# Kernel optimization log

Hardware: AMD Instinct MI355X
Metric: run time of the kernel (lower is better)

The kernel has to match this reference:

```python
import jax, jax.numpy as jnp
import numpy as np

B, C_IN, C_OUT, D, H, W = 2, 128, 128, 16, 32, 32


def setup_inputs() -> dict:
    key = jax.random.key(0)
    kx, kw, kb = jax.random.split(key, 3)
    x = jax.random.normal(kx, (B, C_IN, D, H, W), dtype=jnp.float32)
    # ddpm_conv3x3 -> Conv3d(in_ch, out_ch, kernel=3, padding=1) with default (scaled-variance) init
    fan_in = C_IN * 3 * 3 * 3
    scale = 1.0 / np.sqrt(fan_in)
    Wk = jax.random.uniform(kw, (C_OUT, C_IN, 3, 3, 3), dtype=jnp.float32, minval=-scale, maxval=scale)
    b = jnp.zeros((C_OUT,), dtype=jnp.float32)
    return {"x": x, "Wk": Wk, "b": b}


def reference(x, Wk, b):
    h = jnp.repeat(jnp.repeat(jnp.repeat(x, 2, axis=2), 2, axis=3), 2, axis=4)
    # 3x3x3 conv, stride 1, padding 1 (SAME)
    out = jax.lax.conv_general_dilated(
        h, Wk,
        window_strides=(1, 1, 1),
        padding="SAME",
        dimension_numbers=("NCDHW", "OIDHW", "NCDHW"),
    )
    return out + b[None, :, None, None, None]
```

## Files before the change

### kernel.cpp

```cpp
#include <hip/hip_runtime.h>
#include <hip/hip_bf16.h>

#define B_    2
#define CIN   128
#define COUT  128
#define DD    16
#define HH    32
#define WW    32
#define XS_CI (DD*HH*WW)
#define XS_B  (CIN*XS_CI)
#define OS_H2 64
#define OS_D2 (64*64)
#define OS_CO (32*64*64)
#define OS_B  (COUT*OS_CO)

typedef __attribute__((ext_vector_type(8))) short   short8;
typedef __attribute__((ext_vector_type(4))) float   floatx4;

static __device__ __forceinline__ unsigned short f2bf(float f) {
    union { __hip_bfloat16 h; unsigned short u; } cv;
    cv.h = __float2bfloat16(f);
    return cv.u;
}

__global__ __launch_bounds__(256) void fold_kernel(const float* __restrict__ Wk,
                                                   unsigned short* __restrict__ Afold) {
    const int t = blockIdx.x * 256 + threadIdx.x;
    const int p  = t >> 14;
    const int ks = (t >> 9) & 31;
    const int ct = (t >> 6) & 7;
    const int l  = t & 63;
    const int co = ct * 16 + (l & 15);
    const int ci = ks * 4 + (l >> 4);
    const int ed = (p >> 2) & 1, eh = (p >> 1) & 1, ew = p & 1;

    const float* w = Wk + (co * CIN + ci) * 27;
    float wv[27];
    #pragma unroll
    for (int i = 0; i < 27; ++i) wv[i] = w[i];

    short8 pk;
    #pragma unroll
    for (int tt = 0; tt < 8; ++tt) {
        const int td = (tt >> 2) & 1, th = (tt >> 1) & 1, tw = tt & 1;
        const int dlo = ed ? (td ? 2 : 0) : (td ? 1 : 0);
        const int dhi = ed ? (td ? 2 : 1) : (td ? 2 : 0);
        const int hlo = eh ? (th ? 2 : 0) : (th ? 1 : 0);
        const int hhi = eh ? (th ? 2 : 1) : (th ? 2 : 0);
        const int wlo = ew ? (tw ? 2 : 0) : (tw ? 1 : 0);
        const int whi = ew ? (tw ? 2 : 1) : (tw ? 2 : 0);
        float s = 0.f;
        for (int kd = dlo; kd <= dhi; ++kd)
            for (int kh = hlo; kh <= hhi; ++kh)
                for (int kw = wlo; kw <= whi; ++kw)
                    s += wv[kd * 9 + kh * 3 + kw];
        pk[tt] = (short)f2bf(s);
    }
    reinterpret_cast<short8*>(Afold)[t] = pk;
}

__global__ __launch_bounds__(256) void upconv_mfma(const float* __restrict__ x,
                                                   const unsigned short* __restrict__ Afold,
                                                   const float* __restrict__ bias,
                                                   float* __restrict__ out) {
    __shared__ short Bt[2][128 * 64];
    char* buf0 = reinterpret_cast<char*>(&Bt[0][0]);
    char* buf1 = reinterpret_cast<char*>(&Bt[1][0]);

    const int tid  = threadIdx.x;
    const int wave = tid >> 6;
    const int lane = tid & 63;

    const int d      = blockIdx.x >> 3;
    const int h_base = (blockIdx.x & 7) * 4;
    const int p      = blockIdx.y;
    const int b      = blockIdx.z;
    const int ed = (p >> 2) & 1, eh = (p >> 1) & 1, ew = p & 1;

    const int n_s  = tid & 127;
    const int cils = tid >> 7;
    const int hs   = h_base + (n_s >> 5);
    const int ws_  = n_s & 31;
    const int d0 = d + ed - 1, h0 = hs + eh - 1, w0 = ws_ + ew - 1;

    int  off[8];
    bool ok[8];
    #pragma unroll
    for (int tt = 0; tt < 8; ++tt) {
        const int td = (tt >> 2) & 1, th = (tt >> 1) & 1, tw = tt & 1;
        const int dd2 = d0 + td, hh2 = h0 + th, ww2 = w0 + tw;
        ok[tt]  = ((unsigned)dd2 < DD) && ((unsigned)hh2 < HH) && ((unsigned)ww2 < WW);
        off[tt] = dd2 * (HH * WW) + hh2 * WW + ww2;
    }
    const int sw    = (n_s & 7) << 4;
    const int wbase = n_s * 128;
    const float* xb = x + (size_t)b * XS_B;

    const int co0 = (wave >> 1) * 64;
    const int n0  = (wave & 1) * 64;
    const int ct0 = (wave >> 1) * 4;

    floatx4 acc[4][4];
    #pragma unroll
    for (int i = 0; i < 4; ++i)
        #pragma unroll
        for (int j = 0; j < 4; ++j)
            acc[i][j] = (floatx4){0.f, 0.f, 0.f, 0.f};

    const short8* Ap = reinterpret_cast<const short8*>(Afold);

    float raw[4][8];

    auto gather = [&](int kc) {
        #pragma unroll
        for (int i = 0; i < 4; ++i) {
            const float* xc = xb + (size_t)(kc * 8 + cils + 2 * i) * XS_CI;
            #pragma unroll
            for (int tt = 0; tt < 8; ++tt)
                raw[i][tt] = ok[tt] ? xc[off[tt]] : 0.f;
        }
    };

    auto body = [&](int kc, char* bufc, bool last) {
        short8 a[2][4];
        #pragma unroll
        for (int ksl = 0; ksl < 2; ++ksl)
            #pragma unroll
            for (int ct = 0; ct < 4; ++ct)
                a[ksl][ct] = Ap[((size_t)((p * 32 + kc * 2 + ksl) * 8 + ct0 + ct)) * 64 + lane];

        #pragma unroll
        for (int i = 0; i < 4; ++i) {
            short8 pk;
            #pragma unroll
            for (int tt = 0; tt < 8; ++tt) pk[tt] = (short)f2bf(raw[i][tt]);
            *reinterpret_cast<short8*>(bufc + wbase + (((cils + 2 * i) * 16) ^ sw)) = pk;
        }

        if (!last) gather(kc + 1);

        asm volatile("s_waitcnt lgkmcnt(0)\n\ts_barrier" ::: "memory");

        __builtin_amdgcn_s_setprio(1);
        #pragma unroll
        for (int ksl = 0; ksl < 2; ++ksl) {
            short8 bfr[4];
            #pragma unroll
            for (int nt = 0; nt < 4; ++nt) {
                const int n  = n0 + nt * 16 + (lane & 15);
                const int kb = ksl * 64 + (lane >> 4) * 16;
                bfr[nt] = *reinterpret_cast<const short8*>(
                    bufc + n * 128 + (kb ^ ((n & 7) << 4)));
            }
            #pragma unroll
            for (int ct = 0; ct < 4; ++ct)
                #pragma unroll
                for (int nt = 0; nt < 4; ++nt)
                    acc[ct][nt] = __builtin_amdgcn_mfma_f32_16x16x32_bf16(
                        a[ksl][ct], bfr[nt], acc[ct][nt], 0, 0, 0);
        }
        __builtin_amdgcn_s_setprio(0);
    };

    gather(0);
    for (int kc = 0; kc < 16; kc += 2) {
        body(kc,     buf0, false);
        body(kc + 1, buf1, (kc + 1) == 15);
    }

    float* ob = out + (size_t)b * OS_B + (size_t)(2 * d + ed) * OS_D2;
    #pragma unroll
    for (int ct = 0; ct < 4; ++ct) {
        #pragma unroll
        for (int j = 0; j < 4; ++j) {
            const int co = co0 + ct * 16 + (lane >> 4) * 4 + j;
            const float bv = bias[co];
            #pragma unroll
            for (int nt = 0; nt < 4; ++nt) {
                const int n  = n0 + nt * 16 + (lane & 15);
                const int hl = n >> 5, wl = n & 31;
                const int h2 = 2 * (h_base + hl) + eh;
                const int w2 = 2 * wl + ew;
                ob[(size_t)co * OS_CO + h2 * OS_H2 + w2] = acc[ct][nt][j] + bv;
            }
        }
    }
}

extern "C" void kernel_launch(void* const* d_in, const int* in_sizes, int n_in,
                              void* d_out, int out_size, void* d_ws, size_t ws_size,
                              hipStream_t stream) {
    const float* x    = (const float*)d_in[0];
    const float* Wk   = (const float*)d_in[1];
    const float* bias = (const float*)d_in[2];
    float* out        = (float*)d_out;
    unsigned short* Afold = (unsigned short*)d_ws;

    fold_kernel<<<512, 256, 0, stream>>>(Wk, Afold);
    dim3 grid(DD * 8, 8, B_);
    upconv_mfma<<<grid, 256, 0, stream>>>(x, Afold, bias, out);
}
```

Before: 138.8 us.

## Pre-pad input to bf16 halo buffer and gather with vector loads

Adds a pre-pass that converts x to bf16 into a zero-padded halo buffer in workspace. The main kernel then gathers the 2x2x2 taps with unconditional 32-bit loads, with no per-element bounds checks or fp32-to-bf16 conversion, and repacks pairs into LDS with 128-bit stores. Also precomputes the LDS read addresses and sets launch_bounds occupancy to 3 blocks per CU. In exchange it adds a memset and an extra pad kernel launch, plus a larger workspace footprint.

```diff
diff --git a/kernel.cpp b/kernel.cpp
--- a/kernel.cpp
+++ b/kernel.cpp
@@ -14,13 +14,23 @@
 #define OS_CO (32*64*64)
 #define OS_B  (COUT*OS_CO)
 
-typedef __attribute__((ext_vector_type(8))) short   short8;
-typedef __attribute__((ext_vector_type(4))) float   floatx4;
-
-static __device__ __forceinline__ unsigned short f2bf(float f) {
+#define PD_D  18
+#define PD_H  34
+#define PD_W  36
+#define PD_HW (PD_H*PD_W)
+#define PD_CI (PD_D*PD_HW)
+#define AFOLD_BYTES (8*32*8*64*16)
+#define XPAD_ELEMS  ((size_t)B_*CIN*PD_CI)
+#define XPAD_BYTES  (XPAD_ELEMS*2)
+
+typedef __attribute__((ext_vector_type(8))) short        short8;
+typedef __attribute__((ext_vector_type(4))) float        floatx4;
+typedef __attribute__((ext_vector_type(4))) unsigned int uint4v;
+
+static __device__ __forceinline__ unsigned f2bf(float f) {
     union { __hip_bfloat16 h; unsigned short u; } cv;
     cv.h = __float2bfloat16(f);
-    return cv.u;
+    return (unsigned)cv.u;
 }
 
 __global__ __launch_bounds__(256) void fold_kernel(const float* __restrict__ Wk,
@@ -59,10 +69,26 @@
     reinterpret_cast<short8*>(Afold)[t] = pk;
 }
 
-__global__ __launch_bounds__(256) void upconv_mfma(const float* __restrict__ x,
-                                                   const unsigned short* __restrict__ Afold,
-                                                   const float* __restrict__ bias,
-                                                   float* __restrict__ out) {
+__global__ __launch_bounds__(256) void pad_kernel(const float* __restrict__ x,
+                                                  unsigned* __restrict__ xp32) {
+    const int idx = blockIdx.x * 256 + threadIdx.x;
+    const int w2 = idx & 15;
+    const int h  = (idx >> 4) & 31;
+    const int d  = (idx >> 9) & 15;
+    const int ci = (idx >> 13) & 127;
+    const int b  = (idx >> 20) & 1;
+    const float2 v = *reinterpret_cast<const float2*>(
+        x + (size_t)((b * CIN + ci) * DD + d) * (HH * WW) + h * WW + w2 * 2);
+    xp32[(size_t)((b * CIN + ci) * PD_D + d + 1) * (PD_HW / 2)
+         + (h + 1) * (PD_W / 2) + (w2 + 1)] = f2bf(v.x) | (f2bf(v.y) << 16);
+}
+
+__global__ __launch_bounds__(256, 3) void upconv_mfma(
+    const unsigned short* __restrict__ xp,
+    const unsigned short* __restrict__ Afold,
+    const float* __restrict__ bias,
+    float* __restrict__ out)
+{
     __shared__ short Bt[2][128 * 64];
     char* buf0 = reinterpret_cast<char*>(&Bt[0][0]);
     char* buf1 = reinterpret_cast<char*>(&Bt[1][0]);
@@ -77,28 +103,38 @@
     const int b      = blockIdx.z;
     const int ed = (p >> 2) & 1, eh = (p >> 1) & 1, ew = p & 1;
 
-    const int n_s  = tid & 127;
-    const int cils = tid >> 7;
-    const int hs   = h_base + (n_s >> 5);
-    const int ws_  = n_s & 31;
-    const int d0 = d + ed - 1, h0 = hs + eh - 1, w0 = ws_ + ew - 1;
-
-    int  off[8];
-    bool ok[8];
-    #pragma unroll
-    for (int tt = 0; tt < 8; ++tt) {
-        const int td = (tt >> 2) & 1, th = (tt >> 1) & 1, tw = tt & 1;
-        const int dd2 = d0 + td, hh2 = h0 + th, ww2 = w0 + tw;
-        ok[tt]  = ((unsigned)dd2 < DD) && ((unsigned)hh2 < HH) && ((unsigned)ww2 < WW);
-        off[tt] = dd2 * (HH * WW) + hh2 * WW + ww2;
-    }
-    const int sw    = (n_s & 7) << 4;
-    const int wbase = n_s * 128;
-    const float* xb = x + (size_t)b * XS_B;
+    const int npair = tid & 63;
+    const int grp   = tid >> 6;
+    const int hl    = npair >> 4;
+    const int wlp   = (npair & 15) * 2;
+    const int n_a   = hl * 32 + wlp;
+    const int n_b   = n_a + 1;
+    const int pd  = d + ed;
+    const int ph  = h_base + hl + eh;
+    const int pwb = wlp + 2 * ew;
+    const int roff = pd * PD_HW + ph * PD_W + pwb;
+    const unsigned short* xpb = xp + (size_t)b * CIN * PD_CI;
+
+    int waddr_a[2], waddr_b[2];
+    #pragma unroll
+    for (int i = 0; i < 2; ++i) {
+        const int cl = grp * 2 + i;
+        waddr_a[i] = n_a * 128 + ((cl * 16) ^ ((n_a & 7) << 4));
+        waddr_b[i] = n_b * 128 + ((cl * 16) ^ ((n_b & 7) << 4));
+    }
 
     const int co0 = (wave >> 1) * 64;
     const int n0  = (wave & 1) * 64;
     const int ct0 = (wave >> 1) * 4;
+    int raddr[2][4];
+    #pragma unroll
+    for (int ksl = 0; ksl < 2; ++ksl)
+        #pragma unroll
+        for (int nt = 0; nt < 4; ++nt) {
+            const int n  = n0 + nt * 16 + (lane & 15);
+            const int kb = ksl * 64 + (lane >> 4) * 16;
+            raddr[ksl][nt] = n * 128 + (kb ^ ((n & 7) << 4));
+        }
 
     floatx4 acc[4][4];
     #pragma unroll
@@ -109,15 +145,20 @@
 
     const short8* Ap = reinterpret_cast<const short8*>(Afold);
 
-    float raw[4][8];
-
+    unsigned g[2][4][2];
     auto gather = [&](int kc) {
         #pragma unroll
-        for (int i = 0; i < 4; ++i) {
-            const float* xc = xb + (size_t)(kc * 8 + cils + 2 * i) * XS_CI;
-            #pragma unroll
-            for (int tt = 0; tt < 8; ++tt)
-                raw[i][tt] = ok[tt] ? xc[off[tt]] : 0.f;
+        for (int i = 0; i < 2; ++i) {
+            const char* bc = reinterpret_cast<const char*>(
+                xpb + (size_t)(kc * 8 + grp * 2 + i) * PD_CI + roff);
+            g[i][0][0] = *(const unsigned*)(bc + 0);
+            g[i][0][1] = *(const unsigned*)(bc + 4);
+            g[i][1][0] = *(const unsigned*)(bc + 72);
+            g[i][1][1] = *(const unsigned*)(bc + 76);
+            g[i][2][0] = *(const unsigned*)(bc + 2448);
+            g[i][2][1] = *(const unsigned*)(bc + 2452);
+            g[i][3][0] = *(const unsigned*)(bc + 2520);
+            g[i][3][1] = *(const unsigned*)(bc + 2524);
         }
     };
 
@@ -127,14 +168,20 @@
         for (int ksl = 0; ksl < 2; ++ksl)
             #pragma unroll
             for (int ct = 0; ct < 4; ++ct)
-                a[ksl][ct] = Ap[((size_t)((p * 32 + kc * 2 + ksl) * 8 + ct0 + ct)) * 64 + lane];
-
-        #pragma unroll
-        for (int i = 0; i < 4; ++i) {
-            short8 pk;
-            #pragma unroll
-            for (int tt = 0; tt < 8; ++tt) pk[tt] = (short)f2bf(raw[i][tt]);
-            *reinterpret_cast<short8*>(bufc + wbase + (((cils + 2 * i) * 16) ^ sw)) = pk;
+                a[ksl][ct] = Ap[(size_t)((p * 32 + kc * 2 + ksl) * 8 + ct0 + ct) * 64 + lane];
+
+        #pragma unroll
+        for (int i = 0; i < 2; ++i) {
+            unsigned pa[4], pb[4];
+            #pragma unroll
+            for (int r = 0; r < 4; ++r) {
+                const unsigned l0 = g[i][r][0], l1 = g[i][r][1];
+                const unsigned mid = (l0 >> 16) | (l1 << 16);
+                pa[r] = ew ? l0  : mid;
+                pb[r] = ew ? mid : l1;
+            }
+            *(uint4v*)(bufc + waddr_a[i]) = (uint4v){pa[0], pa[1], pa[2], pa[3]};
+            *(uint4v*)(bufc + waddr_b[i]) = (uint4v){pb[0], pb[1], pb[2], pb[3]};
         }
 
         if (!last) gather(kc + 1);
@@ -146,12 +193,8 @@
         for (int ksl = 0; ksl < 2; ++ksl) {
             short8 bfr[4];
             #pragma unroll
-            for (int nt = 0; nt < 4; ++nt) {
-                const int n  = n0 + nt * 16 + (lane & 15);
-                const int kb = ksl * 64 + (lane >> 4) * 16;
-                bfr[nt] = *reinterpret_cast<const short8*>(
-                    bufc + n * 128 + (kb ^ ((n & 7) << 4)));
-            }
+            for (int nt = 0; nt < 4; ++nt)
+                bfr[nt] = *reinterpret_cast<const short8*>(bufc + raddr[ksl][nt]);
             #pragma unroll
             for (int ct = 0; ct < 4; ++ct)
                 #pragma unroll
@@ -178,8 +221,8 @@
             #pragma unroll
             for (int nt = 0; nt < 4; ++nt) {
                 const int n  = n0 + nt * 16 + (lane & 15);
-                const int hl = n >> 5, wl = n & 31;
-                const int h2 = 2 * (h_base + hl) + eh;
+                const int hh = n >> 5, wl = n & 31;
+                const int h2 = 2 * (h_base + hh) + eh;
                 const int w2 = 2 * wl + ew;
                 ob[(size_t)co * OS_CO + h2 * OS_H2 + w2] = acc[ct][nt][j] + bv;
             }
@@ -194,9 +237,14 @@
     const float* Wk   = (const float*)d_in[1];
     const float* bias = (const float*)d_in[2];
     float* out        = (float*)d_out;
+
     unsigned short* Afold = (unsigned short*)d_ws;
-
+    unsigned short* xpad  = (unsigned short*)((char*)d_ws + AFOLD_BYTES);
+
+    hipMemsetAsync(xpad, 0, XPAD_BYTES, stream);
+    pad_kernel<<<8192, 256, 0, stream>>>(x, (unsigned*)xpad);
     fold_kernel<<<512, 256, 0, stream>>>(Wk, Afold);
+
     dim3 grid(DD * 8, 8, B_);
-    upconv_mfma<<<grid, 256, 0, stream>>>(x, Afold, bias, out);
-}
+    upconv_mfma<<<grid, 256, 0, stream>>>(xpad, Afold, bias, out);
+}
```

After: 114.0 us. 1.22x faster.
